# Kernel optimization log

Measured on AMD Instinct MI355X. Metric: run time of the kernel, lower is better.

## Reference

```python
import jax
import jax.numpy as jnp
import numpy as np
from jax import lax

# Grid / problem dimensions (match init_kwargs / input_specs)
B = 1          # batch_size
D, H, W = 16, 128, 128   # full-resolution voxel grid (z, y, x)
N = 120000     # number of occupied voxels
CIN = 16       # num_input_features
EPS = 1e-5     # MinkowskiBatchNorm eps (eval mode, running stats)


def setup_inputs() -> dict:
    key = jax.random.key(0)
    ks = jax.random.split(key, 24)

    # Unique voxel coordinates (ME.SparseTensor coordinates are unique after quantization)
    perm = jax.random.permutation(ks[0], D * H * W)[:N]
    z = (perm // (H * W)).astype(jnp.int32)
    y = ((perm // W) % H).astype(jnp.int32)
    x = (perm % W).astype(jnp.int32)
    coors = jnp.stack([jnp.zeros(N, jnp.int32), z, y, x], axis=1)  # (batch, z, y, x)

    voxel_features = jax.random.normal(ks[1], (N, CIN), jnp.float32)

    def w(k, shape, fan_in):
        return jax.random.normal(k, shape, jnp.float32) * (1.0 / np.sqrt(fan_in))

    w0 = w(ks[2], (32, 16, 3, 3, 3), 16 * 27)
    w1 = w(ks[3], (32, 32, 3, 3, 3), 32 * 27)
    w2 = w(ks[4], (64, 32, 3, 3, 3), 32 * 27)
    w64 = w(ks[5], (7, 64, 64, 3, 3, 3), 64 * 27)   # the seven 64->64 k=3^3 convs
    w10 = w(ks[6], (64, 64, 3, 1, 1), 64 * 3)        # final k=(3,1,1) conv

    bn32_gamma = 1.0 + 0.1 * jax.random.normal(ks[7], (2, 32), jnp.float32)
    bn32_beta = 0.1 * jax.random.normal(ks[8], (2, 32), jnp.float32)
    bn32_mean = 0.1 * jax.random.normal(ks[9], (2, 32), jnp.float32)
    bn32_var = 0.5 + jax.random.uniform(ks[10], (2, 32), jnp.float32)
    bn64_gamma = 1.0 + 0.1 * jax.random.normal(ks[11], (9, 64), jnp.float32)
    bn64_beta = 0.1 * jax.random.normal(ks[12], (9, 64), jnp.float32)
    bn64_mean = 0.1 * jax.random.normal(ks[13], (9, 64), jnp.float32)
    bn64_var = 0.5 + jax.random.uniform(ks[14], (9, 64), jnp.float32)

    return {
        "voxel_features": voxel_features, "coors": coors,
        "w0": w0, "w1": w1, "w2": w2, "w64": w64, "w10": w10,
        "bn32_gamma": bn32_gamma, "bn32_beta": bn32_beta,
        "bn32_mean": bn32_mean, "bn32_var": bn32_var,
        "bn64_gamma": bn64_gamma, "bn64_beta": bn64_beta,
        "bn64_mean": bn64_mean, "bn64_var": bn64_var,
        "batch_size": B,
    }


def _conv(x, w, stride_z):
    # Minkowski conv with odd kernel is a centered conv; in the z-downsampled
    # dense grid, kernel offsets scaled by tensor stride reduce to ordinary
    # dense conv with 'half' padding per axis and stride on z.
    pads = [(w.shape[2] // 2,) * 2, (w.shape[3] // 2,) * 2, (w.shape[4] // 2,) * 2]
    return lax.conv_general_dilated(
        x, w, (stride_z, 1, 1), pads,
        dimension_numbers=("NCDHW", "OIDHW", "NCDHW"))


def _bn_relu(x, g, b, m, v):
    inv = g / jnp.sqrt(v + EPS)                    # [C]
    sh = (1, -1, 1, 1, 1)
    return jax.nn.relu(x * inv.reshape(sh) + (b - m * inv).reshape(sh))


def _pool_z(occ):
    # strided Minkowski conv output coords = unique(floor(c/2)) of input coords
    return jnp.maximum(occ[:, :, 0::2], occ[:, :, 1::2])


def reference(voxel_features, coors, w0, w1, w2, w64, w10,
              bn32_gamma, bn32_beta, bn32_mean, bn32_var,
              bn64_gamma, bn64_beta, bn64_mean, bn64_var, batch_size):
    b, z, y, x = coors[:, 0], coors[:, 1], coors[:, 2], coors[:, 3]
    # Densify sparse tensor (unoccupied voxels are exact zeros, as in ME)
    h = jnp.zeros((batch_size, D, H, W, CIN), voxel_features.dtype)
    h = h.at[b, z, y, x].set(voxel_features)
    h = jnp.moveaxis(h, -1, 1)                                   # [B,C,D,H,W]
    occ = jnp.zeros((batch_size, 1, D, H, W), voxel_features.dtype)
    occ = occ.at[b, 0, z, y, x].set(1.0)

    # Two 32-channel stride-1 convs: output coords == input coords -> mask with occ
    h = _bn_relu(_conv(h, w0, 1), bn32_gamma[0], bn32_beta[0], bn32_mean[0], bn32_var[0]) * occ
    h = _bn_relu(_conv(h, w1, 1), bn32_gamma[1], bn32_beta[1], bn32_mean[1], bn32_var[1]) * occ

    # 32->64, stride (2,1,1)
    occ = _pool_z(occ)
    h = _bn_relu(_conv(h, w2, 2), bn64_gamma[0], bn64_beta[0], bn64_mean[0], bn64_var[0]) * occ
    # three 64->64 stride-1 convs
    for i in range(3):
        h = _bn_relu(_conv(h, w64[i], 1), bn64_gamma[1 + i], bn64_beta[1 + i], bn64_mean[1 + i], bn64_var[1 + i]) * occ
    # 64->64 stride (2,1,1)
    occ = _pool_z(occ)
    h = _bn_relu(_conv(h, w64[3], 2), bn64_gamma[4], bn64_beta[4], bn64_mean[4], bn64_var[4]) * occ
    # three 64->64 stride-1 convs
    for i in range(3):
        h = _bn_relu(_conv(h, w64[4 + i], 1), bn64_gamma[5 + i], bn64_beta[5 + i], bn64_mean[5 + i], bn64_var[5 + i]) * occ
    # final 64->64, kernel (3,1,1), stride (2,1,1)
    occ = _pool_z(occ)
    h = _bn_relu(_conv(h, w10, 2), bn64_gamma[8], bn64_beta[8], bn64_mean[8], bn64_var[8]) * occ

    # prune is a no-op (all coords in-range by construction); dense() -> [B,C,Dz,H,W]
    n, c, d, hh, ww = h.shape
    return h.reshape(n, c * d, hh, ww)
```

## Files before the change

kernel.cpp:

```cpp
#include <hip/hip_runtime.h>

#define HW 16384

typedef _Float16 half8  __attribute__((ext_vector_type(8)));
typedef _Float16 half4v __attribute__((ext_vector_type(4)));
typedef float    f32x4  __attribute__((ext_vector_type(4)));

typedef __attribute__((address_space(3))) unsigned int lds_u32;
typedef const __attribute__((address_space(1))) unsigned int glb_u32;

__device__ __forceinline__ void gl_lds16(const void* g, void* l) {
    __builtin_amdgcn_global_load_lds((glb_u32*)g, (lds_u32*)l, 16, 0, 0);
}

__global__ void zero4(float4* __restrict__ p, int n4) {
    int i = blockIdx.x * 256 + threadIdx.x;
    if (i < n4) p[i] = make_float4(0.f, 0.f, 0.f, 0.f);
}

__global__ void write_code_f32(float* out, float v) {
    if (threadIdx.x == 0 && blockIdx.x == 0) out[0] = v;
}

__global__ void border_zero(_Float16* __restrict__ base, int D, int CS) {
    int idx = blockIdx.x * 256 + threadIdx.x;
    int gpc = CS / 8;
    int total = D * 516 * gpc;
    if (idx >= total) return;
    int g = idx % gpc;
    int c = (idx / gpc) % 516;
    int d = idx / (gpc * 516);
    int y, x;
    if (c < 130)      { y = 0;           x = c; }
    else if (c < 260) { y = 129;         x = c - 130; }
    else if (c < 388) { y = c - 260 + 1; x = 0; }
    else              { y = c - 388 + 1; x = 129; }
    *(float4*)(base + ((size_t)(d * 130 + y) * 130 + x) * CS + g * 8) =
        make_float4(0.f, 0.f, 0.f, 0.f);
}

struct PackDesc {
    const float* src[11];
    int dstoff[11];
    int cum[12];
    int cinr[11];
    int cinp[11];
    int cout[11];
    int khw[11];
};

__global__ void pack_all(PackDesc pd, _Float16* __restrict__ AP) {
    int u = blockIdx.x * 256 + threadIdx.x;
    if (u >= pd.cum[11]) return;
    int s = 0;
    while (u >= pd.cum[s + 1]) ++s;
    int idx = u - pd.cum[s];
    const int CINr = pd.cinr[s], CINp = pd.cinp[s], KHW = pd.khw[s];
    const int KD = 3;
    const int NSTEPS = KD * KHW * KHW * (CINp / 32);
    const float* W = pd.src[s];
    int lane = idx & 63;
    int st   = (idx >> 6) % NSTEPS;
    int grp  = idx / (NSTEPS * 64);
    int k0  = st * 32 + (lane >> 4) * 8;
    int t   = k0 / CINp;
    int ci0 = k0 % CINp;
    int co  = grp * 16 + (lane & 15);
    int khw2 = KHW * KHW;
    int dz = t / khw2, r = t % khw2, dy = r / KHW, dx = r % KHW;
    half8 hv;
    for (int j = 0; j < 8; ++j) {
        int ci = ci0 + j;
        float wv = (ci < CINr)
            ? W[(((size_t)co * CINr + ci) * KD + dz) * khw2 + dy * KHW + dx] : 0.0f;
        hv[j] = (_Float16)wv;
    }
    *(half8*)(AP + pd.dstoff[s] + ((size_t)(grp * NSTEPS + st) * 64 + lane) * 8) = hv;
}

__global__ void scatter_f16(const float* __restrict__ vf, const int* __restrict__ coors,
                            _Float16* __restrict__ act, unsigned char* __restrict__ occ, int n) {
    int i = blockIdx.x * 256 + threadIdx.x;
    if (i >= n) return;
    int z = coors[i * 4 + 1];
    int y = coors[i * 4 + 2];
    int x = coors[i * 4 + 3];
    size_t cell = ((size_t)(z * 130 + (y + 1)) * 130 + (x + 1)) * 40;
    for (int c = 0; c < 16; ++c) act[cell + c] = (_Float16)vf[i * 16 + c];
    occ[z * HW + y * 128 + x] = 1;
}

__global__ void pool_occ(const unsigned char* __restrict__ o0, unsigned char* __restrict__ o1,
                         unsigned char* __restrict__ o2, unsigned char* __restrict__ o3) {
    int p = blockIdx.x * 256 + threadIdx.x;
    if (p >= HW) return;
    unsigned char a[16];
    for (int z = 0; z < 16; ++z) a[z] = o0[z * HW + p];
    for (int z = 0; z < 8; ++z) { a[z] = a[2 * z] | a[2 * z + 1]; o1[z * HW + p] = a[z]; }
    for (int z = 0; z < 4; ++z) { a[z] = a[2 * z] | a[2 * z + 1]; o2[z * HW + p] = a[z]; }
    for (int z = 0; z < 2; ++z) { a[z] = a[2 * z] | a[2 * z + 1]; o3[z * HW + p] = a[z]; }
}

template <int CINp, int COUT, int KD, int KHW, int SZ, int DIN, int DOUT, bool FINAL>
__global__ __launch_bounds__(512, 4)
void conv_mfma(const _Float16* __restrict__ act, const _Float16* __restrict__ apack,
               const float* __restrict__ gm, const float* __restrict__ bt,
               const float* __restrict__ mn, const float* __restrict__ vr,
               const unsigned char* __restrict__ occ, void* __restrict__ outv) {
    constexpr int PADXY  = KHW / 2;
    constexpr int CB     = CINp / 32;
    constexpr int MGT    = COUT / 16;
    constexpr int MGW    = (MGT + 1) / 2;
    constexpr int NSTEPS = KD * KHW * KHW * CB;
    constexpr int CS     = CINp + 8;
    constexpr int OCS    = COUT + 8;
    constexpr int NGRAN  = 4 * 130 * CS / 8;
    constexpr int NIT    = (NGRAN + 511) / 512;
    constexpr int OFS    = 1 - PADXY;
    constexpr int NWG    = DOUT * 64;

    __shared__ _Float16 smem[4 * 130 * CS];

    const int bid0 = blockIdx.x;
    const int bid = (bid0 & 7) * (NWG / 8) + (bid0 >> 3);
    const int yp = bid & 63;
    const int z0 = bid >> 6;
    const int y0 = yp * 2;
    const int tid  = threadIdx.x;
    const int w    = tid >> 6;
    const int lane = tid & 63;
    const int ylocal = w >> 2;
    const int x0w    = ((w >> 1) & 1) * 64;
    const int chh    = (MGT > 1) ? (w & 1) : 0;
    const int n  = lane & 15;
    const int kg = lane >> 4;

    f32x4 acc[MGW][4];
    #pragma unroll
    for (int m = 0; m < MGW; ++m)
        #pragma unroll
        for (int t = 0; t < 4; ++t) { acc[m][t][0] = 0.f; acc[m][t][1] = 0.f; acc[m][t][2] = 0.f; acc[m][t][3] = 0.f; }

    const int zb = z0 * SZ;
    const int dzlo = (zb == 0) ? 1 : 0;
    const int dzhi = (zb + KD - 1 > DIN) ? (KD - 1) : KD;

    for (int dz = dzlo; dz < dzhi; ++dz) {
        const int zi = zb + dz - 1;
        __syncthreads();
        const _Float16* src = act + (size_t)(zi * 130 + y0) * (130 * CS);
        #pragma unroll
        for (int it = 0; it < NIT; ++it) {
            int g = it * 512 + tid;
            if (g < NGRAN) gl_lds16(src + (size_t)g * 8, smem + (size_t)g * 8);
        }
        asm volatile("s_waitcnt vmcnt(0)" ::: "memory");
        __syncthreads();
        #pragma unroll
        for (int dy = 0; dy < KHW; ++dy) {
            #pragma unroll
            for (int dx = 0; dx < KHW; ++dx) {
                #pragma unroll
                for (int cb = 0; cb < CB; ++cb) {
                    const int sabs = dz * (KHW * KHW * CB) + (dy * KHW + dx) * CB + cb;
                    half8 a[MGW];
                    #pragma unroll
                    for (int mg = 0; mg < MGW; ++mg)
                        a[mg] = *(const half8*)(apack
                            + ((size_t)((chh * MGW + mg) * NSTEPS + sabs) * 64 + lane) * 8);
                    const _Float16* bp = smem
                        + ((ylocal + dy + OFS) * 130 + x0w + n + dx + OFS) * CS + cb * 32 + kg * 8;
                    #pragma unroll
                    for (int nt = 0; nt < 4; ++nt) {
                        half8 b = *(const half8*)(bp + nt * 16 * CS);
                        #pragma unroll
                        for (int mg = 0; mg < MGW; ++mg)
                            acc[mg][nt] = __builtin_amdgcn_mfma_f32_16x16x32_f16(a[mg], b, acc[mg][nt], 0, 0, 0);
                    }
                }
            }
        }
    }

    const int yo = y0 + ylocal;
    #pragma unroll
    for (int mg = 0; mg < MGW; ++mg) {
        const int co0 = (chh * MGW + mg) * 16 + kg * 4;
        const f32x4 gv = *(const f32x4*)(gm + co0);
        const f32x4 bv = *(const f32x4*)(bt + co0);
        const f32x4 mv = *(const f32x4*)(mn + co0);
        const f32x4 vv = *(const f32x4*)(vr + co0);
        float sc[4], sh[4];
        #pragma unroll
        for (int r = 0; r < 4; ++r) {
            sc[r] = gv[r] * __frsqrt_rn(vv[r] + 1e-5f);
            sh[r] = bv[r] - mv[r] * sc[r];
        }
        #pragma unroll
        for (int nt = 0; nt < 4; ++nt) {
            const int x = x0w + nt * 16 + n;
            const float occv = (float)occ[z0 * HW + yo * 128 + x];
            float v0 = fmaxf(fmaf(acc[mg][nt][0], sc[0], sh[0]), 0.f) * occv;
            float v1 = fmaxf(fmaf(acc[mg][nt][1], sc[1], sh[1]), 0.f) * occv;
            float v2 = fmaxf(fmaf(acc[mg][nt][2], sc[2], sh[2]), 0.f) * occv;
            float v3 = fmaxf(fmaf(acc[mg][nt][3], sc[3], sh[3]), 0.f) * occv;
            if constexpr (FINAL) {
                float* o = (float*)outv;
                const int sp = yo * 128 + x;
                o[((size_t)(co0 + 0) * 2 + z0) * HW + sp] = v0;
                o[((size_t)(co0 + 1) * 2 + z0) * HW + sp] = v1;
                o[((size_t)(co0 + 2) * 2 + z0) * HW + sp] = v2;
                o[((size_t)(co0 + 3) * 2 + z0) * HW + sp] = v3;
            } else {
                _Float16* o = (_Float16*)outv;
                half4v hv;
                hv[0] = (_Float16)v0; hv[1] = (_Float16)v1;
                hv[2] = (_Float16)v2; hv[3] = (_Float16)v3;
                *(half4v*)(o + ((size_t)(z0 * 130 + (yo + 1)) * 130 + (x + 1)) * OCS + co0) = hv;
            }
        }
    }
}

extern "C" void kernel_launch(void* const* d_in, const int* in_sizes, int n_in,
                              void* d_out, int out_size, void* d_ws, size_t ws_size,
                              hipStream_t stream) {
    const float* vf    = (const float*)d_in[0];
    const int*   coors = (const int*)d_in[1];
    const float* w0    = (const float*)d_in[2];
    const float* w1    = (const float*)d_in[3];
    const float* w2    = (const float*)d_in[4];
    const float* w64   = (const float*)d_in[5];
    const float* w10   = (const float*)d_in[6];
    const float* g32   = (const float*)d_in[7];
    const float* b32   = (const float*)d_in[8];
    const float* m32   = (const float*)d_in[9];
    const float* v32   = (const float*)d_in[10];
    const float* g64   = (const float*)d_in[11];
    const float* b64   = (const float*)d_in[12];
    const float* m64   = (const float*)d_in[13];
    const float* v64   = (const float*)d_in[14];
    const int N = in_sizes[0] / 16;

    float* out_f = (float*)d_out;

    const size_t R0 = 0;
    const size_t R1 = 21632000;
    const size_t R3 = 43264000;
    const size_t OFF_OCC0 = 62732800;
    const size_t OFF_OCC1 = 62994944;
    const size_t OFF_OCC2 = 63126016;
    const size_t OFF_OCC3 = 63191552;
    const size_t OFF_AP   = 63224320;
    const size_t TOTAL_BYTES = 65018368;

    if (ws_size < TOTAL_BYTES) {
        write_code_f32<<<dim3(1), dim3(64), 0, stream>>>(out_f, 1.0e8f);
        return;
    }

    char* wsb = (char*)d_ws;
    _Float16* A0p = (_Float16*)(wsb + R0);
    _Float16* A1p = (_Float16*)(wsb + R1);
    _Float16* A3p = (_Float16*)(wsb + R3);
    _Float16* A2p = A1p;
    unsigned char* occ0 = (unsigned char*)(wsb + OFF_OCC0);
    unsigned char* occ1 = (unsigned char*)(wsb + OFF_OCC1);
    unsigned char* occ2 = (unsigned char*)(wsb + OFF_OCC2);
    unsigned char* occ3 = (unsigned char*)(wsb + OFF_OCC3);
    _Float16* AP = (_Float16*)(wsb + OFF_AP);

    const size_t W_A0 = 0, W_A1 = 27648, W_A2 = 55296, W_A3 = 110592, W_A10 = 884736;

    zero4<<<dim3((21632000 / 16 + 255) / 256), dim3(256), 0, stream>>>((float4*)(wsb + R0), 21632000 / 16);
    zero4<<<dim3((262144 / 16 + 255) / 256), dim3(256), 0, stream>>>((float4*)occ0, 262144 / 16);
    {
        int t1 = 16 * 516 * (40 / 8);
        border_zero<<<dim3((t1 + 255) / 256), dim3(256), 0, stream>>>(A1p, 16, 40);
        int t3 = 8 * 516 * (72 / 8);
        border_zero<<<dim3((t3 + 255) / 256), dim3(256), 0, stream>>>(A3p, 8, 72);
    }

    {
        PackDesc pd;
        int units[11] = {3456, 3456, 6912, 13824, 13824, 13824, 13824, 13824, 13824, 13824, 1536};
        const float* srcs[11] = {w0, w1, w2,
                                 w64 + 0 * 110592, w64 + 1 * 110592, w64 + 2 * 110592,
                                 w64 + 3 * 110592, w64 + 4 * 110592, w64 + 5 * 110592,
                                 w64 + 6 * 110592, w10};
        int offs[11] = {(int)W_A0, (int)W_A1, (int)W_A2,
                        (int)(W_A3 + 0 * 110592), (int)(W_A3 + 1 * 110592), (int)(W_A3 + 2 * 110592),
                        (int)(W_A3 + 3 * 110592), (int)(W_A3 + 4 * 110592), (int)(W_A3 + 5 * 110592),
                        (int)(W_A3 + 6 * 110592), (int)W_A10};
        int cinr[11] = {16, 32, 32, 64, 64, 64, 64, 64, 64, 64, 64};
        int cinp[11] = {32, 32, 32, 64, 64, 64, 64, 64, 64, 64, 64};
        int cout[11] = {32, 32, 64, 64, 64, 64, 64, 64, 64, 64, 64};
        int khw[11]  = {3, 3, 3, 3, 3, 3, 3, 3, 3, 3, 1};
        int c = 0;
        for (int i = 0; i < 11; ++i) {
            pd.src[i] = srcs[i]; pd.dstoff[i] = offs[i]; pd.cum[i] = c; c += units[i];
            pd.cinr[i] = cinr[i]; pd.cinp[i] = cinp[i]; pd.cout[i] = cout[i]; pd.khw[i] = khw[i];
        }
        pd.cum[11] = c;
        pack_all<<<dim3((c + 255) / 256), dim3(256), 0, stream>>>(pd, AP);
    }

    scatter_f16<<<dim3((N + 255) / 256), dim3(256), 0, stream>>>(vf, coors, A0p, occ0, N);
    pool_occ<<<dim3(HW / 256), dim3(256), 0, stream>>>(occ0, occ1, occ2, occ3);

    conv_mfma<32, 32, 3, 3, 1, 16, 16, false><<<dim3(16 * 64), dim3(512), 0, stream>>>(
        A0p, AP + W_A0, g32, b32, m32, v32, occ0, A1p);
    conv_mfma<32, 32, 3, 3, 1, 16, 16, false><<<dim3(16 * 64), dim3(512), 0, stream>>>(
        A1p, AP + W_A1, g32 + 32, b32 + 32, m32 + 32, v32 + 32, occ0, A0p);
    {
        int t = 8 * 516 * (72 / 8);
        border_zero<<<dim3((t + 255) / 256), dim3(256), 0, stream>>>(A2p, 8, 72);
    }
    conv_mfma<32, 64, 3, 3, 2, 16, 8, false><<<dim3(8 * 64), dim3(512), 0, stream>>>(
        A0p, AP + W_A2, g64, b64, m64, v64, occ1, A2p);
    {
        int t = 4 * 516 * (72 / 8);
        border_zero<<<dim3((t + 255) / 256), dim3(256), 0, stream>>>(A0p, 4, 72);
    }
    conv_mfma<64, 64, 3, 3, 1, 8, 8, false><<<dim3(8 * 64), dim3(512), 0, stream>>>(
        A2p, AP + W_A3 + 0 * 110592, g64 + 64, b64 + 64, m64 + 64, v64 + 64, occ1, A3p);
    conv_mfma<64, 64, 3, 3, 1, 8, 8, false><<<dim3(8 * 64), dim3(512), 0, stream>>>(
        A3p, AP + W_A3 + 1 * 110592, g64 + 128, b64 + 128, m64 + 128, v64 + 128, occ1, A2p);
    conv_mfma<64, 64, 3, 3, 1, 8, 8, false><<<dim3(8 * 64), dim3(512), 0, stream>>>(
        A2p, AP + W_A3 + 2 * 110592, g64 + 192, b64 + 192, m64 + 192, v64 + 192, occ1, A3p);
    conv_mfma<64, 64, 3, 3, 2, 8, 4, false><<<dim3(4 * 64), dim3(512), 0, stream>>>(
        A3p, AP + W_A3 + 3 * 110592, g64 + 256, b64 + 256, m64 + 256, v64 + 256, occ2, A0p);
    {
        int t = 4 * 516 * (72 / 8);
        border_zero<<<dim3((t + 255) / 256), dim3(256), 0, stream>>>(A1p, 4, 72);
    }
    conv_mfma<64, 64, 3, 3, 1, 4, 4, false><<<dim3(4 * 64), dim3(512), 0, stream>>>(
        A0p, AP + W_A3 + 4 * 110592, g64 + 320, b64 + 320, m64 + 320, v64 + 320, occ2, A1p);
    conv_mfma<64, 64, 3, 3, 1, 4, 4, false><<<dim3(4 * 64), dim3(512), 0, stream>>>(
        A1p, AP + W_A3 + 5 * 110592, g64 + 384, b64 + 384, m64 + 384, v64 + 384, occ2, A0p);
    conv_mfma<64, 64, 3, 3, 1, 4, 4, false><<<dim3(4 * 64), dim3(512), 0, stream>>>(
        A0p, AP + W_A3 + 6 * 110592, g64 + 448, b64 + 448, m64 + 448, v64 + 448, occ2, A1p);
    conv_mfma<64, 64, 3, 1, 2, 4, 2, true><<<dim3(2 * 64), dim3(512), 0, stream>>>(
        A1p, AP + W_A10, g64 + 512, b64 + 512, m64 + 512, v64 + 512, occ3, out_f);
}
```

Baseline: 334.6 us.

## Fuse border zeroing into conv epilogue and halve row tile for late layers

Drops the separate border_zero launches and has each non-final conv write zero halo columns and rows for its output tile, so the padded layout stays valid without extra kernels. The workspace is rearranged so occ0 and the first activation buffer are cleared by one zero4 launch. Adds a TR template parameter: the 4-deep layers use one output row per workgroup, with waves split across output channels, which doubles the grid to 512 blocks. The smaller tiles mean each block reloads more halo rows relative to the work it does.

```diff
diff --git a/kernel.cpp b/kernel.cpp
--- a/kernel.cpp
+++ b/kernel.cpp
@@ -20,23 +20,6 @@
 
 __global__ void write_code_f32(float* out, float v) {
     if (threadIdx.x == 0 && blockIdx.x == 0) out[0] = v;
-}
-
-__global__ void border_zero(_Float16* __restrict__ base, int D, int CS) {
-    int idx = blockIdx.x * 256 + threadIdx.x;
-    int gpc = CS / 8;
-    int total = D * 516 * gpc;
-    if (idx >= total) return;
-    int g = idx % gpc;
-    int c = (idx / gpc) % 516;
-    int d = idx / (gpc * 516);
-    int y, x;
-    if (c < 130)      { y = 0;           x = c; }
-    else if (c < 260) { y = 129;         x = c - 130; }
-    else if (c < 388) { y = c - 260 + 1; x = 0; }
-    else              { y = c - 388 + 1; x = 129; }
-    *(float4*)(base + ((size_t)(d * 130 + y) * 130 + x) * CS + g * 8) =
-        make_float4(0.f, 0.f, 0.f, 0.f);
 }
 
 struct PackDesc {
@@ -101,7 +84,7 @@
     for (int z = 0; z < 2; ++z) { a[z] = a[2 * z] | a[2 * z + 1]; o3[z * HW + p] = a[z]; }
 }
 
-template <int CINp, int COUT, int KD, int KHW, int SZ, int DIN, int DOUT, bool FINAL>
+template <int CINp, int COUT, int KD, int KHW, int SZ, int DIN, int DOUT, bool FINAL, int TR = 2>
 __global__ __launch_bounds__(512, 4)
 void conv_mfma(const _Float16* __restrict__ act, const _Float16* __restrict__ apack,
                const float* __restrict__ gm, const float* __restrict__ bt,
@@ -110,28 +93,30 @@
     constexpr int PADXY  = KHW / 2;
     constexpr int CB     = CINp / 32;
     constexpr int MGT    = COUT / 16;
-    constexpr int MGW    = (MGT + 1) / 2;
+    constexpr int MGW    = (TR == 2) ? ((MGT + 1) / 2) : 1;
+    static_assert(TR == 2 || MGT == 4, "TR=1 requires COUT=64");
     constexpr int NSTEPS = KD * KHW * KHW * CB;
     constexpr int CS     = CINp + 8;
     constexpr int OCS    = COUT + 8;
-    constexpr int NGRAN  = 4 * 130 * CS / 8;
+    constexpr int SROWS  = TR + 2;
+    constexpr int NGRAN  = SROWS * 130 * CS / 8;
     constexpr int NIT    = (NGRAN + 511) / 512;
     constexpr int OFS    = 1 - PADXY;
-    constexpr int NWG    = DOUT * 64;
-
-    __shared__ _Float16 smem[4 * 130 * CS];
+    constexpr int NWG    = DOUT * (128 / TR);
+
+    __shared__ _Float16 smem[SROWS * 130 * CS];
 
     const int bid0 = blockIdx.x;
     const int bid = (bid0 & 7) * (NWG / 8) + (bid0 >> 3);
-    const int yp = bid & 63;
-    const int z0 = bid >> 6;
-    const int y0 = yp * 2;
+    const int yp = (TR == 2) ? (bid & 63) : (bid & 127);
+    const int z0 = (TR == 2) ? (bid >> 6) : (bid >> 7);
+    const int y0 = yp * TR;
     const int tid  = threadIdx.x;
     const int w    = tid >> 6;
     const int lane = tid & 63;
-    const int ylocal = w >> 2;
-    const int x0w    = ((w >> 1) & 1) * 64;
-    const int chh    = (MGT > 1) ? (w & 1) : 0;
+    const int ylocal = (TR == 2) ? (w >> 2) : 0;
+    const int x0w    = (TR == 2) ? (((w >> 1) & 1) * 64) : ((w & 1) * 64);
+    const int chsel  = (TR == 2) ? ((MGT > 1) ? (w & 1) : 0) : (w >> 1);
     const int n  = lane & 15;
     const int kg = lane >> 4;
 
@@ -167,7 +152,7 @@
                     #pragma unroll
                     for (int mg = 0; mg < MGW; ++mg)
                         a[mg] = *(const half8*)(apack
-                            + ((size_t)((chh * MGW + mg) * NSTEPS + sabs) * 64 + lane) * 8);
+                            + ((size_t)((chsel * MGW + mg) * NSTEPS + sabs) * 64 + lane) * 8);
                     const _Float16* bp = smem
                         + ((ylocal + dy + OFS) * 130 + x0w + n + dx + OFS) * CS + cb * 32 + kg * 8;
                     #pragma unroll
@@ -185,7 +170,7 @@
     const int yo = y0 + ylocal;
     #pragma unroll
     for (int mg = 0; mg < MGW; ++mg) {
-        const int co0 = (chh * MGW + mg) * 16 + kg * 4;
+        const int co0 = (chsel * MGW + mg) * 16 + kg * 4;
         const f32x4 gv = *(const f32x4*)(gm + co0);
         const f32x4 bv = *(const f32x4*)(bt + co0);
         const f32x4 mv = *(const f32x4*)(mn + co0);
@@ -220,6 +205,36 @@
             }
         }
     }
+
+    if constexpr (!FINAL) {
+        _Float16* o = (_Float16*)outv;
+        constexpr int QC = OCS / 4;
+        half4v zz;
+        zz[0] = (_Float16)0.f; zz[1] = (_Float16)0.f; zz[2] = (_Float16)0.f; zz[3] = (_Float16)0.f;
+        {
+            const int slots = TR * 2 * QC;
+            if (tid < slots) {
+                int q = tid % QC;
+                int c = tid / QC;
+                int r = c >> 1;
+                int side = (c & 1) ? 129 : 0;
+                *(half4v*)(o + ((size_t)(z0 * 130 + (y0 + 1 + r)) * 130 + side) * OCS + q * 4) = zz;
+            }
+        }
+        const int YPMAX = (TR == 2) ? 63 : 127;
+        if (yp == 0) {
+            for (int g = tid; g < 130 * QC; g += 512) {
+                int cell = g / QC, q = g % QC;
+                *(half4v*)(o + ((size_t)(z0 * 130 + 0) * 130 + cell) * OCS + q * 4) = zz;
+            }
+        }
+        if (yp == YPMAX) {
+            for (int g = tid; g < 130 * QC; g += 512) {
+                int cell = g / QC, q = g % QC;
+                *(half4v*)(o + ((size_t)(z0 * 130 + 129) * 130 + cell) * OCS + q * 4) = zz;
+            }
+        }
+    }
 }
 
 extern "C" void kernel_launch(void* const* d_in, const int* in_sizes, int n_in,
@@ -244,10 +259,10 @@
 
     float* out_f = (float*)d_out;
 
-    const size_t R0 = 0;
-    const size_t R1 = 21632000;
-    const size_t R3 = 43264000;
-    const size_t OFF_OCC0 = 62732800;
+    const size_t R0       = 0;
+    const size_t OFF_OCC0 = 21632000;
+    const size_t R1       = 21894144;
+    const size_t R3       = 43526144;
     const size_t OFF_OCC1 = 62994944;
     const size_t OFF_OCC2 = 63126016;
     const size_t OFF_OCC3 = 63191552;
@@ -272,13 +287,9 @@
 
     const size_t W_A0 = 0, W_A1 = 27648, W_A2 = 55296, W_A3 = 110592, W_A10 = 884736;
 
-    zero4<<<dim3((21632000 / 16 + 255) / 256), dim3(256), 0, stream>>>((float4*)(wsb + R0), 21632000 / 16);
-    zero4<<<dim3((262144 / 16 + 255) / 256), dim3(256), 0, stream>>>((float4*)occ0, 262144 / 16);
     {
-        int t1 = 16 * 516 * (40 / 8);
-        border_zero<<<dim3((t1 + 255) / 256), dim3(256), 0, stream>>>(A1p, 16, 40);
-        int t3 = 8 * 516 * (72 / 8);
-        border_zero<<<dim3((t3 + 255) / 256), dim3(256), 0, stream>>>(A3p, 8, 72);
+        const int n4 = (int)((OFF_OCC0 + 262144) / 16);
+        zero4<<<dim3((n4 + 255) / 256), dim3(256), 0, stream>>>((float4*)wsb, n4);
     }
 
     {
@@ -312,33 +323,21 @@
         A0p, AP + W_A0, g32, b32, m32, v32, occ0, A1p);
     conv_mfma<32, 32, 3, 3, 1, 16, 16, false><<<dim3(16 * 64), dim3(512), 0, stream>>>(
         A1p, AP + W_A1, g32 + 32, b32 + 32, m32 + 32, v32 + 32, occ0, A0p);
-    {
-        int t = 8 * 516 * (72 / 8);
-        border_zero<<<dim3((t + 255) / 256), dim3(256), 0, stream>>>(A2p, 8, 72);
-    }
     conv_mfma<32, 64, 3, 3, 2, 16, 8, false><<<dim3(8 * 64), dim3(512), 0, stream>>>(
         A0p, AP + W_A2, g64, b64, m64, v64, occ1, A2p);
-    {
-        int t = 4 * 516 * (72 / 8);
-        border_zero<<<dim3((t + 255) / 256), dim3(256), 0, stream>>>(A0p, 4, 72);
-    }
     conv_mfma<64, 64, 3, 3, 1, 8, 8, false><<<dim3(8 * 64), dim3(512), 0, stream>>>(
         A2p, AP + W_A3 + 0 * 110592, g64 + 64, b64 + 64, m64 + 64, v64 + 64, occ1, A3p);
     conv_mfma<64, 64, 3, 3, 1, 8, 8, false><<<dim3(8 * 64), dim3(512), 0, stream>>>(
         A3p, AP + W_A3 + 1 * 110592, g64 + 128, b64 + 128, m64 + 128, v64 + 128, occ1, A2p);
     conv_mfma<64, 64, 3, 3, 1, 8, 8, false><<<dim3(8 * 64), dim3(512), 0, stream>>>(
         A2p, AP + W_A3 + 2 * 110592, g64 + 192, b64 + 192, m64 + 192, v64 + 192, occ1, A3p);
-    conv_mfma<64, 64, 3, 3, 2, 8, 4, false><<<dim3(4 * 64), dim3(512), 0, stream>>>(
+    conv_mfma<64, 64, 3, 3, 2, 8, 4, false, 1><<<dim3(4 * 128), dim3(512), 0, stream>>>(
         A3p, AP + W_A3 + 3 * 110592, g64 + 256, b64 + 256, m64 + 256, v64 + 256, occ2, A0p);
-    {
-        int t = 4 * 516 * (72 / 8);
-        border_zero<<<dim3((t + 255) / 256), dim3(256), 0, stream>>>(A1p, 4, 72);
-    }
-    conv_mfma<64, 64, 3, 3, 1, 4, 4, false><<<dim3(4 * 64), dim3(512), 0, stream>>>(
+    conv_mfma<64, 64, 3, 3, 1, 4, 4, false, 1><<<dim3(4 * 128), dim3(512), 0, stream>>>(
         A0p, AP + W_A3 + 4 * 110592, g64 + 320, b64 + 320, m64 + 320, v64 + 320, occ2, A1p);
-    conv_mfma<64, 64, 3, 3, 1, 4, 4, false><<<dim3(4 * 64), dim3(512), 0, stream>>>(
+    conv_mfma<64, 64, 3, 3, 1, 4, 4, false, 1><<<dim3(4 * 128), dim3(512), 0, stream>>>(
         A1p, AP + W_A3 + 5 * 110592, g64 + 384, b64 + 384, m64 + 384, v64 + 384, occ2, A0p);
-    conv_mfma<64, 64, 3, 3, 1, 4, 4, false><<<dim3(4 * 64), dim3(512), 0, stream>>>(
+    conv_mfma<64, 64, 3, 3, 1, 4, 4, false, 1><<<dim3(4 * 128), dim3(512), 0, stream>>>(
         A0p, AP + W_A3 + 6 * 110592, g64 + 448, b64 + 448, m64 + 448, v64 + 448, occ2, A1p);
     conv_mfma<64, 64, 3, 1, 2, 4, 2, true><<<dim3(2 * 64), dim3(512), 0, stream>>>(
         A1p, AP + W_A10, g64 + 512, b64 + 512, m64 + 512, v64 + 512, occ3, out_f);
```

Measured after the change: 299.3 us. -10.5%, faster.
